# Optimization experiments

Measured on AMD Instinct MI355X. Metric: run time of the kernel, lower is better.

## Reference

```python
import jax, jax.numpy as jnp
import numpy as np

N = 50000          # total nodes
E_EDGES = 800000   # total edges
G = 8              # graphs in batch
IN_RAW = 16        # raw bus.x columns
X_START, X_END = 4, 10
IN_DIM = X_END - X_START
HID = 256
OUT = 6
NE = 4             # n_experts
K = 2              # top_k
RH = 128           # router hidden
PRIOR_S = 0.35     # size_prior_strength
TEMP = 1.0         # size_temperature
LN_EPS = 1e-5


def setup_inputs() -> dict:
    key = jax.random.key(0)
    ks = jax.random.split(key, 24)
    s = 0.02
    rn = lambda k, shp: jax.random.normal(k, shp, jnp.float32) * s
    inp = {
        "x": jax.random.normal(ks[0], (N, IN_RAW), jnp.float32),
        "edge_index": jax.random.randint(ks[1], (2, E_EDGES), 0, N),
        "batch": jnp.sort(jax.random.randint(ks[2], (N,), 0, G)),
        "num_graphs": G,
        # input encoder: Linear(6,256) -> ReLU -> Linear(256,256)
        "enc_w1": rn(ks[3], (IN_DIM, HID)), "enc_b1": jnp.zeros((HID,), jnp.float32),
        "enc_w2": rn(ks[4], (HID, HID)),   "enc_b2": jnp.zeros((HID,), jnp.float32),
        # router: Linear(256+2,128) -> LayerNorm -> ReLU -> Linear(128,4)
        "rt_w1": rn(ks[5], (HID + 2, RH)), "rt_b1": jnp.zeros((RH,), jnp.float32),
        "ln_g": jnp.ones((RH,), jnp.float32), "ln_b": jnp.zeros((RH,), jnp.float32),
        "rt_w2": rn(ks[6], (RH, NE)),      "rt_b2": jnp.zeros((NE,), jnp.float32),
        "size_centers": jnp.linspace(0.0, 1.0, NE, dtype=jnp.float32),
        # experts: start_conv + 1 mid conv (both HID->HID), stacked [NE, 2, ...]
        "w_rel": rn(ks[7], (NE, 2, HID, HID)), "b_rel": jnp.zeros((NE, 2, HID), jnp.float32),
        "w_root": rn(ks[8], (NE, 2, HID, HID)),
        # end conv HID->OUT
        "w_rel_out": rn(ks[9], (NE, HID, OUT)), "b_rel_out": jnp.zeros((NE, OUT), jnp.float32),
        "w_root_out": rn(ks[10], (NE, HID, OUT)),
    }
    return inp


def _forward(x, edge_index, batch, num_graphs, enc_w1, enc_b1, enc_w2, enc_b2,
             rt_w1, rt_b1, ln_g, ln_b, rt_w2, rt_b2, size_centers,
             w_rel, b_rel, w_root, w_rel_out, b_rel_out, w_root_out):
    n_nodes = x.shape[0]
    src, dst = edge_index[0], edge_index[1]

    # --- input encoder ---
    xs = x[:, X_START:X_END]
    h = jax.nn.relu(xs @ enc_w1 + enc_b1) @ enc_w2 + enc_b2            # [N, HID]

    # --- per-graph size features ---
    ones_n = jnp.ones((n_nodes,), jnp.float32)
    n_per_g = jax.ops.segment_sum(ones_n, batch, num_segments=num_graphs)
    e_per_g = jax.ops.segment_sum(jnp.ones((src.shape[0],), jnp.float32), batch[src], num_segments=num_graphs)
    n_c = jnp.maximum(n_per_g, 1.0)
    log_n = jnp.log(n_c)
    log_e = jnp.log1p(jnp.maximum(e_per_g, 0.0))
    gf = jnp.stack([log_n, log_e], axis=-1)                            # [G, 2]
    gf = (gf - gf.mean(0, keepdims=True)) / (gf.std(0, keepdims=True) + 1e-6)
    log_n_norm = (log_n - log_n.min()) / (log_n.max() - log_n.min() + 1e-6)
    node_feats = gf[batch]                                             # [N, 2]
    node_ln = log_n_norm[batch]                                        # [N]

    # --- router MLP (Linear -> LayerNorm -> ReLU -> Linear) ---
    r = jnp.concatenate([h, node_feats], axis=-1) @ rt_w1 + rt_b1      # [N, RH]
    mu = r.mean(-1, keepdims=True)
    var = ((r - mu) ** 2).mean(-1, keepdims=True)
    r = (r - mu) * jax.lax.rsqrt(var + LN_EPS) * ln_g + ln_b
    learned_logits = jax.nn.relu(r) @ rt_w2 + rt_b2                    # [N, NE]

    # --- deterministic size prior + blend ---
    prior = -((node_ln[:, None] - size_centers[None, :]) ** 2) / max(TEMP, 1e-6)
    logits = (1.0 - PRIOR_S) * learned_logits + PRIOR_S * prior

    # --- sparse top-k gating (eval: no noise) ---
    probs = jax.nn.softmax(logits, axis=-1)                            # [N, NE]
    topv, topi = jax.lax.top_k(probs, K)
    topv = topv / (topv.sum(-1, keepdims=True) + 1e-8)
    rows = jnp.arange(n_nodes)[:, None]
    sw = jnp.zeros_like(probs).at[rows, topi].set(topv)                # [N, NE]

    # --- experts: GraphConv towers; agg_i = sum_{j->i} x_j, out = agg@W_rel + b + x@W_root ---
    agg_h = jax.ops.segment_sum(h[src], dst, num_segments=n_nodes)     # shared first-layer agg
    out = jnp.zeros((n_nodes, OUT), jnp.float32)
    for e in range(NE):
        xe = jax.nn.relu(agg_h @ w_rel[e, 0] + b_rel[e, 0] + h @ w_root[e, 0])
        agg = jax.ops.segment_sum(xe[src], dst, num_segments=n_nodes)
        xe = jax.nn.relu(agg @ w_rel[e, 1] + b_rel[e, 1] + xe @ w_root[e, 1])
        agg = jax.ops.segment_sum(xe[src], dst, num_segments=n_nodes)
        ye = agg @ w_rel_out[e] + b_rel_out[e] + xe @ w_root_out[e]    # [N, OUT]
        out = out + sw[:, e:e + 1] * ye
    return out


def reference(x, edge_index, batch, num_graphs, enc_w1, enc_b1, enc_w2, enc_b2,
              rt_w1, rt_b1, ln_g, ln_b, rt_w2, rt_b2, size_centers,
              w_rel, b_rel, w_root, w_rel_out, b_rel_out, w_root_out):
    return _forward(x, edge_index, batch, num_graphs, enc_w1, enc_b1, enc_w2, enc_b2,
                    rt_w1, rt_b1, ln_g, ln_b, rt_w2, rt_b2, size_centers,
                    w_rel, b_rel, w_root, w_rel_out, b_rel_out, w_root_out)
```

## Files before the change

### kernel.cpp

```cpp
#include <hip/hip_runtime.h>
#include <math.h>

#define N_NODES 50000
#define M_PAD 50048
#define NUM_EDGES 800000
#define NG 8
#define HID 256
#define RHD 128
#define NEXP 4
#define OUTD 6
#define NPW 4
#define SCAN_BLK 196
#define SRS 136

typedef unsigned short bf16_t;
using f32x4  = __attribute__((ext_vector_type(4))) float;
using bf16x8 = __attribute__((ext_vector_type(8))) short;

__device__ __forceinline__ float bf2f(unsigned short u) {
  union { unsigned int i; float f; } v; v.i = ((unsigned int)u) << 16; return v.f;
}
__device__ __forceinline__ unsigned short f2bf(float f) {
  union { float f; unsigned int i; } v; v.f = f;
  unsigned int x = v.i;
  unsigned int r = x + 0x7fffu + ((x >> 16) & 1u);
  return (unsigned short)(r >> 16);
}
__device__ __forceinline__ float readlane_f(float v, int lane) {
  return __int_as_float(__builtin_amdgcn_readlane(__float_as_int(v), lane));
}

__device__ __forceinline__ void gl_lds16(const bf16_t* g, bf16_t* l) {
  __builtin_amdgcn_global_load_lds(
      (const __attribute__((address_space(1))) unsigned int*)(g),
      (__attribute__((address_space(3))) unsigned int*)(l), 16, 0, 0);
}

__global__ void k_zero(int* __restrict__ deg, int* __restrict__ n_cnt,
                       int* __restrict__ e_cnt) {
  int i = blockIdx.x * blockDim.x + threadIdx.x;
  if (i < N_NODES) deg[i] = 0;
  if (i < NG) { n_cnt[i] = 0; e_cnt[i] = 0; }
}

__global__ void k_count(const int* __restrict__ batch, const int* __restrict__ edge,
                        int* __restrict__ n_cnt, int* __restrict__ e_cnt,
                        int* __restrict__ deg) {
  __shared__ int histn[NG], histe[NG];
  int t = threadIdx.x;
  if (t < NG) { histn[t] = 0; histe[t] = 0; }
  __syncthreads();
  int i = blockIdx.x * blockDim.x + t;
  if (i < N_NODES) atomicAdd(&histn[batch[i]], 1);
  if (i < NUM_EDGES) {
    int s = edge[i];
    int d = edge[NUM_EDGES + i];
    atomicAdd(&histe[batch[s]], 1);
    atomicAdd(&deg[d], 1);
  }
  __syncthreads();
  if (t < NG) {
    if (histn[t]) atomicAdd(&n_cnt[t], histn[t]);
    if (histe[t]) atomicAdd(&e_cnt[t], histe[t]);
  }
}

__device__ __forceinline__ float tree8(const float* v) {
  float s01 = __fadd_rn(v[0], v[1]);
  float s23 = __fadd_rn(v[2], v[3]);
  float s45 = __fadd_rn(v[4], v[5]);
  float s67 = __fadd_rn(v[6], v[7]);
  return __fadd_rn(__fadd_rn(s01, s23), __fadd_rn(s45, s67));
}

__global__ void k_graph_stats(const int* __restrict__ n_cnt, const int* __restrict__ e_cnt,
                              float* __restrict__ gf, float* __restrict__ lnn) {
  if (threadIdx.x != 0 || blockIdx.x != 0) return;
  float logn[NG], loge[NG];
  for (int g = 0; g < NG; ++g) {
    float nf = fmaxf((float)n_cnt[g], 1.0f);
    logn[g] = (float)log((double)nf);
    float ef = fmaxf((float)e_cnt[g], 0.0f);
    loge[g] = (float)log1p((double)ef);
  }
  float m0 = __fdiv_rn(tree8(logn), 8.0f);
  float m1 = __fdiv_rn(tree8(loge), 8.0f);
  float sq0[NG], sq1[NG];
  float mn = 3.0e38f, mx = -3.0e38f;
  for (int g = 0; g < NG; ++g) {
    float d0 = __fsub_rn(logn[g], m0);
    float d1 = __fsub_rn(loge[g], m1);
    sq0[g] = __fmul_rn(d0, d0);
    sq1[g] = __fmul_rn(d1, d1);
    mn = fminf(mn, logn[g]); mx = fmaxf(mx, logn[g]);
  }
  float s0 = __fadd_rn(sqrtf(__fdiv_rn(tree8(sq0), 8.0f)), 1e-6f);
  float s1 = __fadd_rn(sqrtf(__fdiv_rn(tree8(sq1), 8.0f)), 1e-6f);
  float denom = __fadd_rn(__fsub_rn(mx, mn), 1e-6f);
  for (int g = 0; g < NG; ++g) {
    gf[g * 2 + 0] = __fdiv_rn(__fsub_rn(logn[g], m0), s0);
    gf[g * 2 + 1] = __fdiv_rn(__fsub_rn(loge[g], m1), s1);
    lnn[g] = __fdiv_rn(__fsub_rn(logn[g], mn), denom);
  }
}

__global__ void k_scan_a(const int* __restrict__ deg, int* __restrict__ excl,
                         int* __restrict__ bsum) {
  __shared__ int temp[256];
  int b = blockIdx.x, t = threadIdx.x;
  int i = b * 256 + t;
  int v = (i < N_NODES) ? deg[i] : 0;
  temp[t] = v;
  __syncthreads();
  for (int off = 1; off < 256; off <<= 1) {
    int x = (t >= off) ? temp[t - off] : 0;
    __syncthreads();
    temp[t] += x;
    __syncthreads();
  }
  if (i < N_NODES) excl[i] = temp[t] - v;
  if (t == 255) bsum[b] = temp[255];
}

__global__ void k_scan_b(const int* __restrict__ bsum, int* __restrict__ boff,
                         int* __restrict__ row_start) {
  __shared__ int temp[256];
  int t = threadIdx.x;
  int v = (t < SCAN_BLK) ? bsum[t] : 0;
  temp[t] = v;
  __syncthreads();
  for (int off = 1; off < 256; off <<= 1) {
    int x = (t >= off) ? temp[t - off] : 0;
    __syncthreads();
    temp[t] += x;
    __syncthreads();
  }
  if (t < SCAN_BLK) boff[t] = temp[t] - v;
  if (t == SCAN_BLK - 1) row_start[N_NODES] = temp[t];
}

__global__ void k_scan_c(const int* __restrict__ excl, const int* __restrict__ boff,
                         int* __restrict__ row_start, int* __restrict__ cursor) {
  int i = blockIdx.x * 256 + threadIdx.x;
  if (i < N_NODES) {
    int e = excl[i] + boff[blockIdx.x];
    row_start[i] = e;
    cursor[i] = e;
  }
}

__global__ void k_fill(const int* __restrict__ edge, int* __restrict__ cursor,
                       int* __restrict__ csr_src) {
  int i = blockIdx.x * blockDim.x + threadIdx.x;
  if (i < NUM_EDGES) {
    int d = edge[NUM_EDGES + i];
    int p = atomicAdd(&cursor[d], 1);
    csr_src[p] = edge[i];
  }
}

__global__ void k_enc1(const float* __restrict__ x, const float* __restrict__ w1,
                       const float* __restrict__ b1, float* __restrict__ t) {
  __shared__ float W[6 * 256];
  __shared__ float xs[16][6];
  int tid = threadIdx.x;
  for (int i = tid; i < 6 * 256; i += 256) W[i] = w1[i];
  int base = blockIdx.x * 16;
  if (tid < 96) {
    int n = tid / 6, k = tid % 6;
    int node = base + n;
    xs[n][k] = (node < N_NODES) ? x[node * 16 + 4 + k] : 0.f;
  }
  __syncthreads();
  float b = b1[tid];
  for (int n = 0; n < 16; ++n) {
    int node = base + n;
    if (node >= N_NODES) break;
    float acc = 0.f;
#pragma unroll
    for (int k = 0; k < 6; ++k) acc = __fmaf_rn(xs[n][k], W[k * 256 + tid], acc);
    t[node * 256 + tid] = fmaxf(__fadd_rn(acc, b), 0.f);
  }
}

__global__ __launch_bounds__(256, 2) void k_gemm_enc(
    const float* __restrict__ A, const float* __restrict__ W0,
    const float* __restrict__ bias, float* __restrict__ C,
    bf16_t* __restrict__ Cb, int M) {
  __shared__ float As[16][132];
  __shared__ float Ws[16][128];
  const int tid = threadIdx.x;
  const int tx = tid & 15;
  const int ty = tid >> 4;
  const int rowBase = blockIdx.x * 128;
  const int colBase = blockIdx.y * 128;

  float acc[2][2][4][4];
#pragma unroll
  for (int a = 0; a < 2; ++a)
#pragma unroll
    for (int b = 0; b < 2; ++b)
#pragma unroll
      for (int i = 0; i < 4; ++i)
#pragma unroll
        for (int j = 0; j < 4; ++j) acc[a][b][i][j] = 0.f;

  for (int kt = 0; kt < 16; ++kt) {
    const int kb = kt * 16;
#pragma unroll
    for (int l = 0; l < 2; ++l) {
      int idx = tid + l * 256;
      int m = idx >> 2;
      int kq = (idx & 3) * 4;
      int arow = rowBase + m;
      float4 av = make_float4(0.f, 0.f, 0.f, 0.f);
      if (arow < M) av = *reinterpret_cast<const float4*>(&A[arow * 256 + kb + kq]);
      As[kq + 0][m] = av.x; As[kq + 1][m] = av.y;
      As[kq + 2][m] = av.z; As[kq + 3][m] = av.w;
    }
#pragma unroll
    for (int l = 0; l < 2; ++l) {
      int idx = tid + l * 256;
      int k = idx >> 5;
      int nq = (idx & 31) * 4;
      float4 wv = *reinterpret_cast<const float4*>(&W0[(kb + k) * 256 + colBase + nq]);
      *reinterpret_cast<float4*>(&Ws[k][nq]) = wv;
    }
    __syncthreads();
#pragma unroll
    for (int k = 0; k < 16; ++k) {
      float4 a0 = *reinterpret_cast<const float4*>(&As[k][ty * 4]);
      float4 a1 = *reinterpret_cast<const float4*>(&As[k][64 + ty * 4]);
      float4 w0 = *reinterpret_cast<const float4*>(&Ws[k][tx * 4]);
      float4 w1 = *reinterpret_cast<const float4*>(&Ws[k][64 + tx * 4]);
      float ar[2][4] = {{a0.x, a0.y, a0.z, a0.w}, {a1.x, a1.y, a1.z, a1.w}};
      float wr[2][4] = {{w0.x, w0.y, w0.z, w0.w}, {w1.x, w1.y, w1.z, w1.w}};
#pragma unroll
      for (int ri = 0; ri < 2; ++ri)
#pragma unroll
        for (int i = 0; i < 4; ++i)
#pragma unroll
          for (int ci = 0; ci < 2; ++ci)
#pragma unroll
            for (int j = 0; j < 4; ++j)
              acc[ri][ci][i][j] = __fmaf_rn(ar[ri][i], wr[ci][j], acc[ri][ci][i][j]);
    }
    __syncthreads();
  }
  float4 bv0 = *reinterpret_cast<const float4*>(&bias[colBase + tx * 4]);
  float4 bv1 = *reinterpret_cast<const float4*>(&bias[colBase + 64 + tx * 4]);
  float bb[2][4] = {{bv0.x, bv0.y, bv0.z, bv0.w}, {bv1.x, bv1.y, bv1.z, bv1.w}};
#pragma unroll
  for (int ri = 0; ri < 2; ++ri) {
#pragma unroll
    for (int i = 0; i < 4; ++i) {
      int row = rowBase + ri * 64 + ty * 4 + i;
      if (row < M) {
#pragma unroll
        for (int ci = 0; ci < 2; ++ci) {
          float o[4];
#pragma unroll
          for (int j = 0; j < 4; ++j)
            o[j] = __fadd_rn(acc[ri][ci][i][j], bb[ci][j]);
          *reinterpret_cast<float4*>(&C[row * 256 + colBase + ci * 64 + tx * 4]) =
              make_float4(o[0], o[1], o[2], o[3]);
          ushort4 ob = make_ushort4(f2bf(o[0]), f2bf(o[1]), f2bf(o[2]), f2bf(o[3]));
          *reinterpret_cast<ushort4*>(&Cb[(size_t)row * 256 + colBase + ci * 64 + tx * 4]) = ob;
        }
      }
    }
  }
}

__global__ void k_wprep(const float* __restrict__ w_rel, const float* __restrict__ w_root,
                        bf16_t* __restrict__ WT) {
  __shared__ bf16_t tile[64][258];
  int m = blockIdx.x;
  int k0 = blockIdx.y * 64;
  const float* src = (m < 8) ? (w_rel + (size_t)m * 65536)
                             : (w_root + (size_t)(m - 8) * 65536);
  bf16_t* dst = WT + (size_t)m * 65536;
  int tid = threadIdx.x;
  for (int r = 0; r < 64; ++r)
    tile[r][tid] = f2bf(src[(k0 + r) * 256 + tid]);
  __syncthreads();
  for (int c = 0; c < 64; c += 8) {
    ushort4 lo, hi;
    lo.x = tile[c + 0][tid]; lo.y = tile[c + 1][tid];
    lo.z = tile[c + 2][tid]; lo.w = tile[c + 3][tid];
    hi.x = tile[c + 4][tid]; hi.y = tile[c + 5][tid];
    hi.z = tile[c + 6][tid]; hi.w = tile[c + 7][tid];
    *reinterpret_cast<ushort4*>(&dst[tid * 256 + k0 + c]) = lo;
    *reinterpret_cast<ushort4*>(&dst[tid * 256 + k0 + c + 4]) = hi;
  }
}

__device__ __forceinline__ void gemm_core128(
    const bf16_t* __restrict__ A, const bf16_t* __restrict__ W0t,
    const bf16_t* __restrict__ B, const bf16_t* __restrict__ W1t,
    const float* __restrict__ bias, bf16_t* __restrict__ C, int rowBase) {
  __shared__ bf16_t As[128 * 64];
  __shared__ bf16_t Bs[256 * 64];
  const int tid = threadIdx.x;
  const int lane = tid & 63;
  const int wave = tid >> 6;
  const int lm = lane & 15;
  const int quad = lane >> 4;
  const int wn = wave * 64;
  const int lrow = lane >> 3;
  const int lslot = lane & 7;

  f32x4 acc[8][4];
#pragma unroll
  for (int i = 0; i < 8; ++i)
#pragma unroll
    for (int j = 0; j < 4; ++j) acc[i][j] = (f32x4){0.f, 0.f, 0.f, 0.f};

#pragma unroll
  for (int phase = 0; phase < 2; ++phase) {
    const bf16_t* __restrict__ Ain = phase ? B : A;
    const bf16_t* __restrict__ Wt  = phase ? W1t : W0t;
    for (int kc = 0; kc < 4; ++kc) {
      const int kb = kc * 64;
#pragma unroll
      for (int l = 0; l < 4; ++l) {
        int s = wave * 4 + l;
        int row = s * 8 + lrow;
        int srcc = kb + ((lslot ^ (row & 7)) << 3);
        gl_lds16(&Ain[(size_t)(rowBase + row) * 256 + srcc], &As[s * 512]);
      }
#pragma unroll
      for (int l = 0; l < 8; ++l) {
        int s = wave * 8 + l;
        int row = s * 8 + lrow;
        int srcc = kb + ((lslot ^ (row & 7)) << 3);
        gl_lds16(&Wt[(size_t)row * 256 + srcc], &Bs[s * 512]);
      }
      __syncthreads();
#pragma unroll
      for (int k2 = 0; k2 < 2; ++k2) {
        const int c0 = k2 * 32 + quad * 8;
        bf16x8 af[8], bfr[4];
#pragma unroll
        for (int i = 0; i < 8; ++i) {
          int ar = i * 16 + lm;
          af[i] = *reinterpret_cast<const bf16x8*>(&As[ar * 64 + (c0 ^ ((ar & 7) << 3))]);
        }
#pragma unroll
        for (int j = 0; j < 4; ++j) {
          int br = wn + j * 16 + lm;
          bfr[j] = *reinterpret_cast<const bf16x8*>(&Bs[br * 64 + (c0 ^ ((br & 7) << 3))]);
        }
#pragma unroll
        for (int i = 0; i < 8; ++i)
#pragma unroll
          for (int j = 0; j < 4; ++j)
            acc[i][j] = __builtin_amdgcn_mfma_f32_16x16x32_bf16(af[i], bfr[j], acc[i][j], 0, 0, 0);
      }
      __syncthreads();
    }
  }
  float bj[4];
#pragma unroll
  for (int j = 0; j < 4; ++j) bj[j] = bias[wn + j * 16 + lm];
#pragma unroll
  for (int i = 0; i < 8; ++i) {
#pragma unroll
    for (int j = 0; j < 4; ++j) {
      int col = wn + j * 16 + lm;
#pragma unroll
      for (int r = 0; r < 4; ++r) {
        int row = rowBase + i * 16 + quad * 4 + r;
        C[(size_t)row * 256 + col] = f2bf(fmaxf(acc[i][j][r] + bj[j], 0.f));
      }
    }
  }
}

__global__ __launch_bounds__(256, 2) void k_gemm1_b(
    const bf16_t* __restrict__ AGG, const bf16_t* __restrict__ hb,
    const bf16_t* __restrict__ WT, const float* __restrict__ b_rel,
    bf16_t* __restrict__ X1p, int pe) {
  int slot = blockIdx.y, e = pe + slot;
  gemm_core128(AGG, WT + (size_t)(e * 2) * 65536,
               hb, WT + (size_t)(8 + e * 2) * 65536,
               b_rel + (size_t)(e * 2) * 256,
               X1p + (size_t)slot * M_PAD * 256, blockIdx.x * 128);
}

__global__ __launch_bounds__(256, 2) void k_gemm2_b(
    const bf16_t* __restrict__ A1p, bf16_t* __restrict__ X1p,
    const bf16_t* __restrict__ WT, const float* __restrict__ b_rel, int pe) {
  int slot = blockIdx.y, e = pe + slot;
  bf16_t* Xs = X1p + (size_t)slot * M_PAD * 256;
  gemm_core128(A1p + (size_t)slot * M_PAD * 256, WT + (size_t)(e * 2 + 1) * 65536,
               Xs, WT + (size_t)(8 + e * 2 + 1) * 65536,
               b_rel + (size_t)(e * 2 + 1) * 256, Xs, blockIdx.x * 128);
}

__device__ __forceinline__ void gather_core(
    const int* __restrict__ row_start, const int* __restrict__ csr_src,
    const bf16_t* __restrict__ X, bf16_t* __restrict__ Cout) {
  int tid = threadIdx.x;
  int r = blockIdx.x * 8 + (tid >> 5);
  int f = (tid & 31) * 8;
  int j0 = row_start[r], j1 = row_start[r + 1];
  float a[8] = {0.f, 0.f, 0.f, 0.f, 0.f, 0.f, 0.f, 0.f};
  int j = j0;
  for (; j + 3 < j1; j += 4) {
    int s0 = csr_src[j];
    int s1 = csr_src[j + 1];
    int s2 = csr_src[j + 2];
    int s3 = csr_src[j + 3];
    bf16x8 v0 = *reinterpret_cast<const bf16x8*>(&X[(size_t)s0 * 256 + f]);
    bf16x8 v1 = *reinterpret_cast<const bf16x8*>(&X[(size_t)s1 * 256 + f]);
    bf16x8 v2 = *reinterpret_cast<const bf16x8*>(&X[(size_t)s2 * 256 + f]);
    bf16x8 v3 = *reinterpret_cast<const bf16x8*>(&X[(size_t)s3 * 256 + f]);
#pragma unroll
    for (int t = 0; t < 8; ++t) a[t] += bf2f((unsigned short)v0[t]);
#pragma unroll
    for (int t = 0; t < 8; ++t) a[t] += bf2f((unsigned short)v1[t]);
#pragma unroll
    for (int t = 0; t < 8; ++t) a[t] += bf2f((unsigned short)v2[t]);
#pragma unroll
    for (int t = 0; t < 8; ++t) a[t] += bf2f((unsigned short)v3[t]);
  }
  for (; j < j1; ++j) {
    int s = csr_src[j];
    bf16x8 v = *reinterpret_cast<const bf16x8*>(&X[(size_t)s * 256 + f]);
#pragma unroll
    for (int t = 0; t < 8; ++t) a[t] += bf2f((unsigned short)v[t]);
  }
  ushort4 lo = make_ushort4(f2bf(a[0]), f2bf(a[1]), f2bf(a[2]), f2bf(a[3]));
  ushort4 hi = make_ushort4(f2bf(a[4]), f2bf(a[5]), f2bf(a[6]), f2bf(a[7]));
  *reinterpret_cast<ushort4*>(&Cout[(size_t)r * 256 + f]) = lo;
  *reinterpret_cast<ushort4*>(&Cout[(size_t)r * 256 + f + 4]) = hi;
}

__global__ void k_gather(const int* __restrict__ row_start, const int* __restrict__ csr_src,
                         const bf16_t* __restrict__ X, bf16_t* __restrict__ Cout) {
  gather_core(row_start, csr_src, X, Cout);
}

__global__ void k_gather_b(const int* __restrict__ row_start, const int* __restrict__ csr_src,
                           const bf16_t* __restrict__ X1p, bf16_t* __restrict__ A1p) {
  size_t off = (size_t)blockIdx.y * M_PAD * 256;
  gather_core(row_start, csr_src, X1p + off, A1p + off);
}

__global__ __launch_bounds__(256) void k_router_np(
    const float* __restrict__ h, const int* __restrict__ batch,
    const float* __restrict__ gf, const float* __restrict__ lnn,
    const float* __restrict__ rtw1, const float* __restrict__ rtb1,
    const float* __restrict__ lng, const float* __restrict__ lnb,
    const float* __restrict__ rtw2, const float* __restrict__ rtb2,
    const float* __restrict__ centers, float* __restrict__ sw) {
  __shared__ float smem[4][1104];
  const int tid = threadIdx.x;
  const int w = tid >> 6;
  const int l = tid & 63;
  const int nbase = blockIdx.x * (4 * NPW) + w * NPW;
  float* sm = smem[w];

#pragma unroll
  for (int j = 0; j < 4; ++j) {
    f32x4 v;
#pragma unroll
    for (int nn = 0; nn < NPW; ++nn)
      v[nn] = h[(size_t)(nbase + nn) * 256 + j * 64 + l];
    *reinterpret_cast<f32x4*>(&sm[(j * 64 + l) * 4]) = v;
  }
  __syncthreads();

  float acc0[NPW], acc1[NPW];
#pragma unroll
  for (int nn = 0; nn < NPW; ++nn) { acc0[nn] = 0.f; acc1[nn] = 0.f; }
#pragma unroll
  for (int j = 0; j < 4; ++j) {
#pragma unroll 16
    for (int k2 = 0; k2 < 64; ++k2) {
      int k = j * 64 + k2;
      float w0 = rtw1[k * RHD + l];
      float w1 = rtw1[k * RHD + l + 64];
      f32x4 hv = *reinterpret_cast<const f32x4*>(&sm[k * 4]);
#pragma unroll
      for (int nn = 0; nn < NPW; ++nn) {
        acc0[nn] = __fmaf_rn(hv[nn], w0, acc0[nn]);
        acc1[nn] = __fmaf_rn(hv[nn], w1, acc1[nn]);
      }
    }
  }

  float g0a = rtw1[256 * RHD + l],      g1a = rtw1[257 * RHD + l];
  float g0b = rtw1[256 * RHD + l + 64], g1b = rtw1[257 * RHD + l + 64];
  float b0 = rtb1[l], b1v = rtb1[l + 64];
  float lga = lng[l], lgb = lng[l + 64];
  float lba = lnb[l], lbb = lnb[l + 64];

  float r0[NPW], r1[NPW];
#pragma unroll
  for (int nn = 0; nn < NPW; ++nn) {
    int node = nbase + nn;
    int g = batch[node];
    float gf0 = gf[g * 2 + 0], gf1 = gf[g * 2 + 1];
    float t0 = acc0[nn], t1 = acc1[nn];
    t0 = __fmaf_rn(gf0, g0a, t0);
    t0 = __fmaf_rn(gf1, g1a, t0);
    t1 = __fmaf_rn(gf0, g0b, t1);
    t1 = __fmaf_rn(gf1, g1b, t1);
    r0[nn] = __fadd_rn(t0, b0);
    r1[nn] = __fadd_rn(t1, b1v);
    sm[nn * SRS + l] = r0[nn];
    sm[nn * SRS + 64 + l] = r1[nn];
  }
  __syncthreads();

  float aj = 0.f;
  if (l < 32) {
    const float* Sp = &sm[(l >> 3) * SRS];
    int rj = l & 7;
    aj = Sp[rj];
    for (int i = 8; i < 128; i += 8) aj = __fadd_rn(aj, Sp[i + rj]);
  }
  float mu[NPW];
#pragma unroll
  for (int nn = 0; nn < NPW; ++nn) {
    float a0 = __shfl(aj, nn * 8 + 0, 64), a1 = __shfl(aj, nn * 8 + 1, 64);
    float a2 = __shfl(aj, nn * 8 + 2, 64), a3 = __shfl(aj, nn * 8 + 3, 64);
    float a4 = __shfl(aj, nn * 8 + 4, 64), a5 = __shfl(aj, nn * 8 + 5, 64);
    float a6 = __shfl(aj, nn * 8 + 6, 64), a7 = __shfl(aj, nn * 8 + 7, 64);
    float s01 = __fadd_rn(a0, a1), s23 = __fadd_rn(a2, a3);
    float s45 = __fadd_rn(a4, a5), s67 = __fadd_rn(a6, a7);
    float t = __fadd_rn(__fadd_rn(s01, s23), __fadd_rn(s45, s67));
    mu[nn] = __fdiv_rn(t, 128.0f);
  }

  float d0[NPW], d1[NPW];
#pragma unroll
  for (int nn = 0; nn < NPW; ++nn) {
    d0[nn] = __fsub_rn(r0[nn], mu[nn]);
    d1[nn] = __fsub_rn(r1[nn], mu[nn]);
    sm[nn * SRS + l] = __fmul_rn(d0[nn], d0[nn]);
    sm[nn * SRS + 64 + l] = __fmul_rn(d1[nn], d1[nn]);
  }
  __syncthreads();

  float qj = 0.f;
  if (l < 32) {
    const float* Sp = &sm[(l >> 3) * SRS];
    int rj = l & 7;
    qj = Sp[rj];
    for (int i = 8; i < 128; i += 8) qj = __fadd_rn(qj, Sp[i + rj]);
  }
#pragma unroll
  for (int nn = 0; nn < NPW; ++nn) {
    float a0 = __shfl(qj, nn * 8 + 0, 64), a1 = __shfl(qj, nn * 8 + 1, 64);
    float a2 = __shfl(qj, nn * 8 + 2, 64), a3 = __shfl(qj, nn * 8 + 3, 64);
    float a4 = __shfl(qj, nn * 8 + 4, 64), a5 = __shfl(qj, nn * 8 + 5, 64);
    float a6 = __shfl(qj, nn * 8 + 6, 64), a7 = __shfl(qj, nn * 8 + 7, 64);
    float s01 = __fadd_rn(a0, a1), s23 = __fadd_rn(a2, a3);
    float s45 = __fadd_rn(a4, a5), s67 = __fadd_rn(a6, a7);
    float t = __fadd_rn(__fadd_rn(s01, s23), __fadd_rn(s45, s67));
    float var = __fdiv_rn(t, 128.0f);
    float inv = __fdiv_rn(1.0f, sqrtf(__fadd_rn(var, 1e-5f)));
    float y0 = __fadd_rn(__fmul_rn(__fmul_rn(d0[nn], inv), lga), lba);
    float y1 = __fadd_rn(__fmul_rn(__fmul_rn(d1[nn], inv), lgb), lbb);
    sm[544 + nn * SRS + l] = fmaxf(y0, 0.f);
    sm[544 + nn * SRS + 64 + l] = fmaxf(y1, 0.f);
  }
  __syncthreads();

  if (l < 16) {
    int nn = l >> 2, c = l & 3;
    int node = nbase + nn;
    const float* Ap = &sm[544 + nn * SRS];
    float acc = 0.f;
    for (int k = 0; k < 128; ++k) acc = __fmaf_rn(Ap[k], rtw2[k * 4 + c], acc);
    float lrn = __fadd_rn(acc, rtb2[c]);
    float nl = lnn[batch[node]];
    float dd = __fsub_rn(nl, centers[c]);
    float pr = -__fmul_rn(dd, dd);
    sm[1088 + nn * 4 + c] = __fadd_rn(__fmul_rn(0.65f, lrn), __fmul_rn(0.35f, pr));
  }
  __syncthreads();

  if (l < NPW) {
    int nn = l;
    int node = nbase + nn;
    float lg[4] = {sm[1088 + nn * 4 + 0], sm[1088 + nn * 4 + 1],
                   sm[1088 + nn * 4 + 2], sm[1088 + nn * 4 + 3]};
    float mx = fmaxf(fmaxf(lg[0], lg[1]), fmaxf(lg[2], lg[3]));
    float e[4];
#pragma unroll
    for (int c = 0; c < 4; ++c)
      e[c] = (float)exp((double)__fsub_rn(lg[c], mx));
    float S = __fadd_rn(__fadd_rn(__fadd_rn(e[0], e[1]), e[2]), e[3]);
    float p[4];
#pragma unroll
    for (int c = 0; c < 4; ++c) p[c] = __fdiv_rn(e[c], S);
    int i1 = 0;
#pragma unroll
    for (int c = 1; c < 4; ++c) if (p[c] > p[i1]) i1 = c;
    int i2 = -1;
#pragma unroll
    for (int c = 0; c < 4; ++c) {
      if (c == i1) continue;
      if (i2 < 0 || p[c] > p[i2]) i2 = c;
    }
    float den = __fadd_rn(__fadd_rn(p[i1], p[i2]), 1e-8f);
    float swv[4] = {0.f, 0.f, 0.f, 0.f};
    swv[i1] = __fdiv_rn(p[i1], den);
    swv[i2] = __fdiv_rn(p[i2], den);
    *reinterpret_cast<float4*>(&sw[node * 4]) =
        make_float4(swv[0], swv[1], swv[2], swv[3]);
  }
}

__global__ void k_headPQ_b(const bf16_t* __restrict__ X2p,
                           const float* __restrict__ w_relo, const float* __restrict__ w_rooto,
                           float* __restrict__ Pp, float* __restrict__ Qp, int pe) {
  int slot = blockIdx.y, e = pe + slot;
  const bf16_t* X2 = X2p + (size_t)slot * M_PAD * 256;
  const float* wro = w_relo + (size_t)e * 256 * OUTD;
  const float* wto = w_rooto + (size_t)e * 256 * OUTD;
  int tid = threadIdx.x;
  int r = blockIdx.x * 4 + (tid >> 6);
  int lane = tid & 63;
  int k0 = lane * 4;
  float wr_[24], wt_[24];
#pragma unroll
  for (int q = 0; q < 6; ++q) {
    float4 a = *reinterpret_cast<const float4*>(&wro[k0 * 6 + q * 4]);
    wr_[q * 4 + 0] = a.x; wr_[q * 4 + 1] = a.y; wr_[q * 4 + 2] = a.z; wr_[q * 4 + 3] = a.w;
    float4 b = *reinterpret_cast<const float4*>(&wto[k0 * 6 + q * 4]);
    wt_[q * 4 + 0] = b.x; wt_[q * 4 + 1] = b.y; wt_[q * 4 + 2] = b.z; wt_[q * 4 + 3] = b.w;
  }
  ushort4 xv4 = *reinterpret_cast<const ushort4*>(&X2[(size_t)r * 256 + k0]);
  float xv[4] = {bf2f(xv4.x), bf2f(xv4.y), bf2f(xv4.z), bf2f(xv4.w)};
  float p[12] = {0.f, 0.f, 0.f, 0.f, 0.f, 0.f, 0.f, 0.f, 0.f, 0.f, 0.f, 0.f};
#pragma unroll
  for (int jj = 0; jj < 4; ++jj)
#pragma unroll
    for (int c = 0; c < 6; ++c) {
      p[c]     += xv[jj] * wr_[jj * 6 + c];
      p[6 + c] += xv[jj] * wt_[jj * 6 + c];
    }
#pragma unroll
  for (int off = 32; off > 0; off >>= 1)
#pragma unroll
    for (int c = 0; c < 12; ++c) p[c] += __shfl_down(p[c], off, 64);
  if (lane == 0) {
#pragma unroll
    for (int c = 0; c < 6; ++c) {
      Pp[(size_t)r * 32 + e * 8 + c] = p[c];
      Qp[(size_t)r * 32 + e * 8 + c] = p[6 + c];
    }
  }
}

__global__ void k_headfin_all(const int* __restrict__ row_start,
                              const int* __restrict__ csr_src,
                              const float* __restrict__ Pp, const float* __restrict__ Qp,
                              const float* __restrict__ b_relo,
                              const float* __restrict__ sw, float* __restrict__ out) {
  int tid = threadIdx.x;
  int r = blockIdx.x * 8 + (tid >> 5);
  int l32 = tid & 31;
  int e = l32 >> 3, c = l32 & 7;
  int j0 = row_start[r], j1 = row_start[r + 1];
  float av = 0.f;
  int j = j0;
  for (; j + 3 < j1; j += 4) {
    int s0 = csr_src[j];
    int s1 = csr_src[j + 1];
    int s2 = csr_src[j + 2];
    int s3 = csr_src[j + 3];
    float v0 = Pp[(size_t)s0 * 32 + l32];
    float v1 = Pp[(size_t)s1 * 32 + l32];
    float v2 = Pp[(size_t)s2 * 32 + l32];
    float v3 = Pp[(size_t)s3 * 32 + l32];
    av += v0; av += v1; av += v2; av += v3;
  }
  for (; j < j1; ++j) av += Pp[(size_t)csr_src[j] * 32 + l32];
  float q = Qp[(size_t)r * 32 + l32];
  float b = (c < 6) ? b_relo[e * 6 + c] : 0.f;
  float t = av + b + q;
  int base = tid & 32;
  float t0 = __shfl(t, base + c, 64);
  float t1 = __shfl(t, base + 8 + c, 64);
  float t2 = __shfl(t, base + 16 + c, 64);
  float t3 = __shfl(t, base + 24 + c, 64);
  if (e == 0 && c < 6) {
    float4 s4 = *reinterpret_cast<const float4*>(&sw[r * 4]);
    float v = s4.x * t0;
    v += s4.y * t1;
    v += s4.z * t2;
    v += s4.w * t3;
    out[r * 6 + c] = v;
  }
}

extern "C" void kernel_launch(void* const* d_in, const int* in_sizes, int n_in,
                              void* d_out, int out_size, void* d_ws, size_t ws_size,
                              hipStream_t stream) {
  const float* x        = (const float*)d_in[0];
  const int*   edge     = (const int*)d_in[1];
  const int*   batch    = (const int*)d_in[2];
  const float* enc_w1   = (const float*)d_in[4];
  const float* enc_b1   = (const float*)d_in[5];
  const float* enc_w2   = (const float*)d_in[6];
  const float* enc_b2   = (const float*)d_in[7];
  const float* rt_w1    = (const float*)d_in[8];
  const float* rt_b1    = (const float*)d_in[9];
  const float* ln_g     = (const float*)d_in[10];
  const float* ln_b     = (const float*)d_in[11];
  const float* rt_w2    = (const float*)d_in[12];
  const float* rt_b2    = (const float*)d_in[13];
  const float* centers  = (const float*)d_in[14];
  const float* w_rel    = (const float*)d_in[15];
  const float* b_rel    = (const float*)d_in[16];
  const float* w_root   = (const float*)d_in[17];
  const float* w_relo   = (const float*)d_in[18];
  const float* b_relo   = (const float*)d_in[19];
  const float* w_rooto  = (const float*)d_in[20];
  float* out = (float*)d_out;

  char* wsp = (char*)d_ws;
  auto alloc = [&](size_t bytes) -> char* {
    char* p = wsp;
    wsp += (bytes + 255) & ~(size_t)255;
    return p;
  };
  const size_t actF32 = (size_t)M_PAD * 256 * sizeof(float);
  const size_t actB16 = (size_t)M_PAD * 256 * sizeof(bf16_t);
  char*   hx  = alloc(actF32);
  float*  h   = (float*)hx;
  bf16_t* X1p = (bf16_t*)hx;
  char*   tx  = alloc(actF32);
  float*  t   = (float*)tx;
  bf16_t* A1p = (bf16_t*)tx;
  bf16_t* hb  = (bf16_t*)alloc(actB16);
  bf16_t* AGG = (bf16_t*)alloc(actB16);
  bf16_t* WT  = (bf16_t*)alloc((size_t)16 * 65536 * sizeof(bf16_t));
  float* Pp   = (float*)alloc((size_t)N_NODES * 32 * sizeof(float));
  float* Qp   = (float*)alloc((size_t)N_NODES * 32 * sizeof(float));
  float* swp  = (float*)alloc((size_t)N_NODES * 4 * sizeof(float));
  int*   n_cnt = (int*)alloc(NG * sizeof(int));
  int*   e_cnt = (int*)alloc(NG * sizeof(int));
  float* gfbuf = (float*)alloc(NG * 2 * sizeof(float));
  float* lnn   = (float*)alloc(NG * sizeof(float));
  int* deg       = (int*)alloc((size_t)N_NODES * sizeof(int));
  int* row_start = (int*)alloc((size_t)(N_NODES + 1) * sizeof(int));
  int* cursor    = (int*)alloc((size_t)N_NODES * sizeof(int));
  int* excl      = (int*)alloc((size_t)N_NODES * sizeof(int));
  int* bsum      = (int*)alloc(SCAN_BLK * sizeof(int));
  int* boff      = (int*)alloc(SCAN_BLK * sizeof(int));
  int* csr_src   = (int*)alloc((size_t)NUM_EDGES * sizeof(int));

  k_zero<<<(N_NODES + 255) / 256, 256, 0, stream>>>(deg, n_cnt, e_cnt);
  k_count<<<(NUM_EDGES + 255) / 256, 256, 0, stream>>>(batch, edge, n_cnt, e_cnt, deg);
  k_graph_stats<<<1, 64, 0, stream>>>(n_cnt, e_cnt, gfbuf, lnn);
  k_scan_a<<<SCAN_BLK, 256, 0, stream>>>(deg, excl, bsum);
  k_scan_b<<<1, 256, 0, stream>>>(bsum, boff, row_start);
  k_scan_c<<<SCAN_BLK, 256, 0, stream>>>(excl, boff, row_start, cursor);
  k_fill<<<(NUM_EDGES + 255) / 256, 256, 0, stream>>>(edge, cursor, csr_src);
  dim3 wgrid(16, 4);
  k_wprep<<<wgrid, 256, 0, stream>>>(w_rel, w_root, WT);

  k_enc1<<<(N_NODES + 15) / 16, 256, 0, stream>>>(x, enc_w1, enc_b1, t);
  dim3 egrid(M_PAD / 128, 2);
  k_gemm_enc<<<egrid, 256, 0, stream>>>(t, enc_w2, enc_b2, h, hb, N_NODES);

  k_router_np<<<N_NODES / (4 * NPW), 256, 0, stream>>>(
      h, batch, gfbuf, lnn, rt_w1, rt_b1, ln_g, ln_b, rt_w2, rt_b2, centers, swp);

  k_gather<<<N_NODES / 8, 256, 0, stream>>>(row_start, csr_src, hb, AGG);

  dim3 ggrid(M_PAD / 128, 2);
  dim3 grid_gather(N_NODES / 8, 2);
  dim3 grid_pq(N_NODES / 4, 2);
  for (int pe = 0; pe < NEXP; pe += 2) {
    k_gemm1_b<<<ggrid, 256, 0, stream>>>(AGG, hb, WT, b_rel, X1p, pe);
    k_gather_b<<<grid_gather, 256, 0, stream>>>(row_start, csr_src, X1p, A1p);
    k_gemm2_b<<<ggrid, 256, 0, stream>>>(A1p, X1p, WT, b_rel, pe);
    k_headPQ_b<<<grid_pq, 256, 0, stream>>>(X1p, w_relo, w_rooto, Pp, Qp, pe);
  }
  k_headfin_all<<<N_NODES / 8, 256, 0, stream>>>(
      row_start, csr_src, Pp, Qp, b_relo, swp, out);
}
```

Baseline: 1.013 ms.

## Fuse first encoder layer into encoder GEMM A-tile load

Removes the separate k_enc1 kernel that wrote a 50000x256 fp32 intermediate, and instead computes relu(x[:,4:10]@W1+b1) on the fly while filling the shared-memory A tile of the second encoder GEMM. The K tile is also enlarged from 16 to 64, cutting the number of k-iterations and barriers. This avoids writing and reading back about 51 MB of intermediate data. In exchange it uses more shared memory (about 75 KB per block), which may limit occupancy under launch_bounds(256,2). The first-layer math is also recomputed once per column block (two times in total).

```diff
diff --git a/kernel.cpp b/kernel.cpp
--- a/kernel.cpp
+++ b/kernel.cpp
@@ -159,42 +159,33 @@
   }
 }
 
-__global__ void k_enc1(const float* __restrict__ x, const float* __restrict__ w1,
-                       const float* __restrict__ b1, float* __restrict__ t) {
-  __shared__ float W[6 * 256];
-  __shared__ float xs[16][6];
-  int tid = threadIdx.x;
-  for (int i = tid; i < 6 * 256; i += 256) W[i] = w1[i];
-  int base = blockIdx.x * 16;
-  if (tid < 96) {
-    int n = tid / 6, k = tid % 6;
-    int node = base + n;
-    xs[n][k] = (node < N_NODES) ? x[node * 16 + 4 + k] : 0.f;
-  }
-  __syncthreads();
-  float b = b1[tid];
-  for (int n = 0; n < 16; ++n) {
-    int node = base + n;
-    if (node >= N_NODES) break;
-    float acc = 0.f;
-#pragma unroll
-    for (int k = 0; k < 6; ++k) acc = __fmaf_rn(xs[n][k], W[k * 256 + tid], acc);
-    t[node * 256 + tid] = fmaxf(__fadd_rn(acc, b), 0.f);
-  }
-}
-
 __global__ __launch_bounds__(256, 2) void k_gemm_enc(
-    const float* __restrict__ A, const float* __restrict__ W0,
-    const float* __restrict__ bias, float* __restrict__ C,
-    bf16_t* __restrict__ Cb, int M) {
-  __shared__ float As[16][132];
-  __shared__ float Ws[16][128];
+    const float* __restrict__ x, const float* __restrict__ w1,
+    const float* __restrict__ b1,
+    const float* __restrict__ W0, const float* __restrict__ bias,
+    float* __restrict__ C, bf16_t* __restrict__ Cb, int M) {
+  __shared__ float As[64][132];
+  __shared__ float Ws[64][128];
+  __shared__ float xs[128][6];
+  __shared__ float w1s[6 * 256];
+  __shared__ float b1s[256];
   const int tid = threadIdx.x;
   const int tx = tid & 15;
   const int ty = tid >> 4;
   const int rowBase = blockIdx.x * 128;
   const int colBase = blockIdx.y * 128;
 
+#pragma unroll
+  for (int l = 0; l < 3; ++l) {
+    int idx = tid + l * 256;
+    int n = idx / 6, j = idx % 6;
+    int node = rowBase + n;
+    xs[n][j] = (node < M) ? x[node * 16 + 4 + j] : 0.f;
+  }
+#pragma unroll
+  for (int l = 0; l < 6; ++l) w1s[tid + l * 256] = w1[tid + l * 256];
+  b1s[tid] = b1[tid];
+
   float acc[2][2][4][4];
 #pragma unroll
   for (int a = 0; a < 2; ++a)
@@ -205,21 +196,30 @@
 #pragma unroll
         for (int j = 0; j < 4; ++j) acc[a][b][i][j] = 0.f;
 
-  for (int kt = 0; kt < 16; ++kt) {
-    const int kb = kt * 16;
-#pragma unroll
-    for (int l = 0; l < 2; ++l) {
-      int idx = tid + l * 256;
-      int m = idx >> 2;
-      int kq = (idx & 3) * 4;
-      int arow = rowBase + m;
-      float4 av = make_float4(0.f, 0.f, 0.f, 0.f);
-      if (arow < M) av = *reinterpret_cast<const float4*>(&A[arow * 256 + kb + kq]);
-      As[kq + 0][m] = av.x; As[kq + 1][m] = av.y;
-      As[kq + 2][m] = av.z; As[kq + 3][m] = av.w;
-    }
-#pragma unroll
-    for (int l = 0; l < 2; ++l) {
+  __syncthreads();
+
+  for (int kt = 0; kt < 4; ++kt) {
+    const int kb = kt * 64;
+    {
+      int m = tid & 127;
+      int kh = tid >> 7;
+      int node = rowBase + m;
+#pragma unroll
+      for (int k2 = 0; k2 < 32; ++k2) {
+        int k = kh * 32 + k2;
+        float a = 0.f;
+        if (node < M) {
+          float accv = 0.f;
+#pragma unroll
+          for (int j = 0; j < 6; ++j)
+            accv = __fmaf_rn(xs[m][j], w1s[j * 256 + kb + k], accv);
+          a = fmaxf(__fadd_rn(accv, b1s[kb + k]), 0.f);
+        }
+        As[k][m] = a;
+      }
+    }
+#pragma unroll
+    for (int l = 0; l < 8; ++l) {
       int idx = tid + l * 256;
       int k = idx >> 5;
       int nq = (idx & 31) * 4;
@@ -227,14 +227,14 @@
       *reinterpret_cast<float4*>(&Ws[k][nq]) = wv;
     }
     __syncthreads();
-#pragma unroll
-    for (int k = 0; k < 16; ++k) {
+#pragma unroll 8
+    for (int k = 0; k < 64; ++k) {
       float4 a0 = *reinterpret_cast<const float4*>(&As[k][ty * 4]);
       float4 a1 = *reinterpret_cast<const float4*>(&As[k][64 + ty * 4]);
       float4 w0 = *reinterpret_cast<const float4*>(&Ws[k][tx * 4]);
-      float4 w1 = *reinterpret_cast<const float4*>(&Ws[k][64 + tx * 4]);
+      float4 w1v = *reinterpret_cast<const float4*>(&Ws[k][64 + tx * 4]);
       float ar[2][4] = {{a0.x, a0.y, a0.z, a0.w}, {a1.x, a1.y, a1.z, a1.w}};
-      float wr[2][4] = {{w0.x, w0.y, w0.z, w0.w}, {w1.x, w1.y, w1.z, w1.w}};
+      float wr[2][4] = {{w0.x, w0.y, w0.z, w0.w}, {w1v.x, w1v.y, w1v.z, w1v.w}};
 #pragma unroll
       for (int ri = 0; ri < 2; ++ri)
 #pragma unroll
@@ -737,7 +737,6 @@
   float*  h   = (float*)hx;
   bf16_t* X1p = (bf16_t*)hx;
   char*   tx  = alloc(actF32);
-  float*  t   = (float*)tx;
   bf16_t* A1p = (bf16_t*)tx;
   bf16_t* hb  = (bf16_t*)alloc(actB16);
   bf16_t* AGG = (bf16_t*)alloc(actB16);
@@ -767,9 +766,9 @@
   dim3 wgrid(16, 4);
   k_wprep<<<wgrid, 256, 0, stream>>>(w_rel, w_root, WT);
 
-  k_enc1<<<(N_NODES + 15) / 16, 256, 0, stream>>>(x, enc_w1, enc_b1, t);
   dim3 egrid(M_PAD / 128, 2);
-  k_gemm_enc<<<egrid, 256, 0, stream>>>(t, enc_w2, enc_b2, h, hb, N_NODES);
+  k_gemm_enc<<<egrid, 256, 0, stream>>>(x, enc_w1, enc_b1, enc_w2, enc_b2,
+                                        h, hb, N_NODES);
 
   k_router_np<<<N_NODES / (4 * NPW), 256, 0, stream>>>(
       h, batch, gfbuf, lnn, rt_w1, rt_b1, ln_g, ln_b, rt_w2, rt_b2, centers, swp);
```

Result: no change. 1.009 ms (-0.4%).
